# Kernel optimization log

Measured on AMD Instinct MI355X. Metric: run time of the kernel, lower is better.

## Reference

```python
import jax, jax.numpy as jnp
import numpy as np

N = 50000   # nodes
E = 400000  # edges
IN = 32     # in_channel
M = 64      # mid_channel
L = 3       # num_layers
EPS = 1e-5


def layer_norm(x, g, b):
    mu = jnp.mean(x, axis=-1, keepdims=True)
    var = jnp.mean((x - mu) ** 2, axis=-1, keepdims=True)
    return (x - mu) / jnp.sqrt(var + EPS) * g + b


def setup_inputs() -> dict:
    key = jax.random.key(0)
    ks = jax.random.split(key, 14)
    s = 0.05
    return {
        "x": jax.random.normal(ks[0], (N, IN), jnp.float32),
        "edge_index": jax.random.randint(ks[1], (2, E), 0, N, jnp.int64),
        # node encoder: Linear(IN->M) + LayerNorm(M)
        "enc_W": jax.random.normal(ks[2], (IN, M), jnp.float32) * s,
        "enc_b": jnp.zeros((M,), jnp.float32),
        "enc_g": jnp.ones((M,), jnp.float32),
        "enc_beta": jnp.zeros((M,), jnp.float32),
        # per-layer pre-norm
        "ln_g": jnp.ones((L, M), jnp.float32),
        "ln_b": jnp.zeros((L, M), jnp.float32),
        # SAGEConvV2 edge MLP: Linear(2M->2M) -> ReLU -> Linear(2M->M)
        "W1": jax.random.normal(ks[3], (L, 2 * M, 2 * M), jnp.float32) * s,
        "b1": jnp.zeros((L, 2 * M), jnp.float32),
        "W2": jax.random.normal(ks[4], (L, 2 * M, M), jnp.float32) * s,
        "b2": jnp.zeros((L, M), jnp.float32),
        # root weight lin_r: Linear(M->M, bias=False)
        "Wr": jax.random.normal(ks[5], (L, M, M), jnp.float32) * s,
    }


def reference(x, edge_index, enc_W, enc_b, enc_g, enc_beta,
              ln_g, ln_b, W1, b1, W2, b2, Wr):
    src = edge_index[0]  # x_j source nodes
    dst = edge_index[1]  # x_i target nodes (aggregation index)
    # node encoder
    x = layer_norm(x @ enc_W + enc_b, enc_g, enc_beta)
    # mean-aggregation denominator (in-degree, clamped to 1 like PyG scatter-mean)
    deg = jax.ops.segment_sum(jnp.ones((E,), x.dtype), dst, num_segments=N)
    deg = jnp.maximum(deg, 1.0)[:, None]
    for l in range(L):  # small fixed layer count
        # res+ block: norm -> act -> (dropout: identity in eval) -> conv -> residual
        h = jax.nn.relu(layer_norm(x, ln_g[l], ln_b[l]))
        # message: concat([x_i, x_j]) -> 2-layer MLP   [E, 2M] -> [E, M]
        msg = jnp.concatenate([h[dst], h[src]], axis=-1)
        msg = jax.nn.relu(msg @ W1[l] + b1[l]) @ W2[l] + b2[l]
        # scatter-mean aggregate at target nodes
        agg = jax.ops.segment_sum(msg, dst, num_segments=N) / deg
        # root weight
        h = agg + h @ Wr[l]
        x = x + h
    return x
```

## Files before the change

kernel.cpp:

```cpp
#include <hip/hip_runtime.h>
#include <hip/hip_bf16.h>

#define N_NODES 50000
#define N_EDGES 400000
#define IN_CH 32
#define EPS 1e-5f
#define SCAN_NB ((N_NODES + 1023) / 1024)
#define EL_CAP 384

#define HIST_B ((N_EDGES + 255) / 256)
#define WCT_TOT (3 * 320 * 64)
#define W2T_TOT (3 * 64 * 128)
#define RPK_B ((WCT_TOT + W2T_TOT + 255) / 256)
#define ENC_B ((N_NODES + 3) / 4)

typedef __attribute__((ext_vector_type(8))) short bh8;
typedef __attribute__((ext_vector_type(4))) float fx4;
typedef __attribute__((ext_vector_type(2))) float fx2;

static __device__ __forceinline__ unsigned int f2bf(float f) {
    __hip_bfloat16 h = __float2bfloat16(f);
    return (unsigned int)*(unsigned short*)&h;
}
static __device__ __forceinline__ unsigned short f2bfu(float f) {
    __hip_bfloat16 h = __float2bfloat16(f);
    return *(unsigned short*)&h;
}
static __device__ __forceinline__ float bflo(unsigned int u) { return __uint_as_float(u << 16); }

__global__ __launch_bounds__(256) void setup_kernel(
    const int* __restrict__ ei, int* __restrict__ cnt,
    const float* __restrict__ W1, const float* __restrict__ Wr,
    const float* __restrict__ W2,
    unsigned short* __restrict__ WcT, unsigned short* __restrict__ W2T,
    const float* __restrict__ x, const float* __restrict__ encW,
    const float* __restrict__ encb, const float* __restrict__ encg,
    const float* __restrict__ encbeta, float* __restrict__ xout) {
    int b = blockIdx.x;
    if (b < HIST_B) {
        int e = b * 256 + threadIdx.x;
        if (e < N_EDGES) atomicAdd(&cnt[ei[N_EDGES + e]], 1);
        return;
    }
    b -= HIST_B;
    if (b < RPK_B) {
        int t = b * 256 + threadIdx.x;
        if (t < WCT_TOT) {
            int l = t / (320 * 64);
            int rem = t % (320 * 64);
            int j = rem / 64, c = rem % 64;
            float v;
            if (j < 128)      v = W1[(l * 128 + c) * 128 + j];
            else if (j < 256) v = W1[(l * 128 + 64 + c) * 128 + (j - 128)];
            else              v = Wr[(l * 64 + c) * 64 + (j - 256)];
            WcT[t] = f2bfu(v);
        } else if (t < WCT_TOT + W2T_TOT) {
            int t2 = t - WCT_TOT;
            int l = t2 / 8192, rem = t2 % 8192;
            int n = rem / 128, k = rem % 128;
            W2T[t2] = f2bfu(W2[l * 8192 + k * 64 + n]);
        }
        return;
    }
    b -= RPK_B;
    __shared__ float wlds[IN_CH * 64];
    for (int t = threadIdx.x; t < IN_CH * 64; t += 256) wlds[t] = encW[t];
    __syncthreads();
    int lane = threadIdx.x & 63;
    int node = b * 4 + (threadIdx.x >> 6);
    if (node >= N_NODES) return;
    float xv = (lane < IN_CH) ? x[node * IN_CH + lane] : 0.f;
    float acc = encb[lane];
    #pragma unroll
    for (int c = 0; c < IN_CH; ++c) {
        float xc = __shfl(xv, c, 64);
        acc += xc * wlds[c * 64 + lane];
    }
    float s = acc;
    for (int off = 32; off; off >>= 1) s += __shfl_xor(s, off, 64);
    float mu = s * (1.f / 64.f);
    float d = acc - mu;
    float q = d * d;
    for (int off = 32; off; off >>= 1) q += __shfl_xor(q, off, 64);
    float r = rsqrtf(q * (1.f / 64.f) + EPS);
    xout[node * 64 + lane] = d * r * encg[lane] + encbeta[lane];
}

__global__ __launch_bounds__(1024) void scan1_kernel(const int* __restrict__ cnt,
                                                     int* __restrict__ exw,
                                                     int* __restrict__ bsum) {
    int b = blockIdx.x, t = threadIdx.x;
    int i = b * 1024 + t;
    int v = (i < N_NODES) ? cnt[i] : 0;
    int lane = t & 63, w = t >> 6;
    int s = v;
    #pragma unroll
    for (int off = 1; off < 64; off <<= 1) {
        int u = __shfl_up(s, off, 64);
        if (lane >= off) s += u;
    }
    __shared__ int ws[16];
    if (lane == 63) ws[w] = s;
    __syncthreads();
    if (t < 16) {
        int sv = ws[t];
        #pragma unroll
        for (int off = 1; off < 16; off <<= 1) {
            int u = __shfl_up(sv, off, 64);
            if (lane >= off) sv += u;
        }
        ws[t] = sv;
    }
    __syncthreads();
    int prefix = (w > 0) ? ws[w - 1] : 0;
    int incl = s + prefix;
    if (i < N_NODES) exw[i] = incl - v;
    if (t == 1023) bsum[b] = incl;
}

__global__ __launch_bounds__(1024) void scan3_kernel(const int* __restrict__ exw,
                                                     const int* __restrict__ bsum,
                                                     int* __restrict__ rp,
                                                     int* __restrict__ cnt) {
    __shared__ int pfx;
    __shared__ int total;
    int b = blockIdx.x, t = threadIdx.x;
    if (t < 64) {
        int v = (t < SCAN_NB) ? bsum[t] : 0;
        #pragma unroll
        for (int off = 1; off < 64; off <<= 1) {
            int u = __shfl_up(v, off, 64);
            if (t >= off) v += u;
        }
        if (b == 0 && t == 0) pfx = 0;
        if (b > 0 && t == b - 1) pfx = v;
        if (t == SCAN_NB - 1) total = v;
    }
    __syncthreads();
    int i = b * 1024 + t;
    if (i < N_NODES) {
        rp[i] = exw[i] + pfx;
        cnt[i] = 0;
    }
    if (b == 0 && t == 0) rp[N_NODES] = total;
}

__global__ void fill_kernel(const int* __restrict__ ei, const int* __restrict__ rp,
                            int* __restrict__ cur, int* __restrict__ el) {
    int e = blockIdx.x * 256 + threadIdx.x;
    if (e < N_EDGES) {
        int d = ei[N_EDGES + e];
        int p = atomicAdd(&cur[d], 1);
        el[rp[d] + p] = ei[e];
    }
}

__global__ __launch_bounds__(256, 8) void fused8_kernel(
    float* __restrict__ x,
    const unsigned char* __restrict__ A8I, const unsigned char* __restrict__ B8I,
    const unsigned short* __restrict__ W2T, const float* __restrict__ b2,
    const int* __restrict__ rp, const int* __restrict__ el,
    const float* __restrict__ g, const float* __restrict__ bvec,
    const unsigned short* __restrict__ WcT, const float* __restrict__ b1,
    unsigned char* __restrict__ A8O, unsigned char* __restrict__ B8O,
    unsigned short* __restrict__ Rbf, int mode) {
    __shared__ float bufF[1088];
    __shared__ unsigned int slds[16][68];
    __shared__ int el_lds[EL_CAP];
    __shared__ int rp_lds[17];
    int tid = threadIdx.x;
    int lane = tid & 63, wid = tid >> 6;
    int l15 = lane & 15, g4 = lane >> 4;
    int base = blockIdx.x * 16;
    unsigned int* hU = (unsigned int*)bufF;
    int n = tid >> 4, sq = tid & 15;

    int col = wid * 16 + l15;
    int nd_l = base + g4 * 4;

    if (mode != 0) {
        if (tid < 17) rp_lds[tid] = rp[min(base + tid, N_NODES)];
        __syncthreads();
        int e0 = rp_lds[0];
        int nE = rp_lds[16] - e0;
        bool inl = (nE <= EL_CAP);
        if (inl) for (int t = tid; t < nE; t += 256) el_lds[t] = el[e0 + t];

        int nd_g = base + n;
        float av[8], acc[8];
        {
            uint2 a0 = *(const uint2*)(A8I + (size_t)min(nd_g, N_NODES - 1) * 128 + sq * 8);
            fx2 d0 = __builtin_amdgcn_cvt_pk_f32_fp8((int)a0.x, false);
            fx2 d1 = __builtin_amdgcn_cvt_pk_f32_fp8((int)a0.x, true);
            fx2 d2 = __builtin_amdgcn_cvt_pk_f32_fp8((int)a0.y, false);
            fx2 d3 = __builtin_amdgcn_cvt_pk_f32_fp8((int)a0.y, true);
            av[0] = d0.x; av[1] = d0.y; av[2] = d1.x; av[3] = d1.y;
            av[4] = d2.x; av[5] = d2.y; av[6] = d3.x; av[7] = d3.y;
        }
        #pragma unroll
        for (int i = 0; i < 8; ++i) acc[i] = 0.f;

        float xpre[4], rpre[4];
        #pragma unroll
        for (int r = 0; r < 4; ++r) {
            int nd = min(nd_l + r, N_NODES - 1);
            xpre[r] = x[(size_t)nd * 64 + col];
            rpre[r] = bflo((unsigned int)Rbf[(size_t)nd * 64 + col]);
        }
        __syncthreads();

        int es = rp_lds[n] - e0, ee = rp_lds[n + 1] - e0;
        int e2 = es;
        int cn = ee - e2; if (cn > 8) cn = 8;
        uint2 bufv[8];
        #pragma unroll
        for (int j = 0; j < 8; ++j)
            if (j < cn) {
                int src = inl ? el_lds[e2 + j] : el[e0 + e2 + j];
                bufv[j] = *(const uint2*)(B8I + (size_t)src * 128 + sq * 8);
            }
        while (cn > 0) {
            #pragma unroll
            for (int j = 0; j < 8; ++j)
                if (j < cn) {
                    fx2 f0 = __builtin_amdgcn_cvt_pk_f32_fp8((int)bufv[j].x, false);
                    fx2 f1 = __builtin_amdgcn_cvt_pk_f32_fp8((int)bufv[j].x, true);
                    fx2 f2 = __builtin_amdgcn_cvt_pk_f32_fp8((int)bufv[j].y, false);
                    fx2 f3 = __builtin_amdgcn_cvt_pk_f32_fp8((int)bufv[j].y, true);
                    acc[0] += fmaxf(av[0] + f0.x, 0.f);
                    acc[1] += fmaxf(av[1] + f0.y, 0.f);
                    acc[2] += fmaxf(av[2] + f1.x, 0.f);
                    acc[3] += fmaxf(av[3] + f1.y, 0.f);
                    acc[4] += fmaxf(av[4] + f2.x, 0.f);
                    acc[5] += fmaxf(av[5] + f2.y, 0.f);
                    acc[6] += fmaxf(av[6] + f3.x, 0.f);
                    acc[7] += fmaxf(av[7] + f3.y, 0.f);
                }
            e2 += cn;
            cn = ee - e2; if (cn > 8) cn = 8;
            #pragma unroll
            for (int j = 0; j < 8; ++j)
                if (j < cn) {
                    int src = inl ? el_lds[e2 + j] : el[e0 + e2 + j];
                    bufv[j] = *(const uint2*)(B8I + (size_t)src * 128 + sq * 8);
                }
        }
        #pragma unroll
        for (int jj = 0; jj < 4; ++jj)
            slds[n][sq * 4 + jj] = f2bf(acc[2 * jj]) | (f2bf(acc[2 * jj + 1]) << 16);
        __syncthreads();

        bh8 sa[4];
        #pragma unroll
        for (int ks = 0; ks < 4; ++ks)
            sa[ks] = *(const bh8*)&slds[l15][ks * 16 + g4 * 4];
        fx4 accm = (fx4){0.f, 0.f, 0.f, 0.f};
        #pragma unroll
        for (int ks = 0; ks < 4; ++ks) {
            bh8 bf = *(const bh8*)(W2T + ((size_t)(wid * 16 + l15) * 128 + ks * 32 + g4 * 8));
            accm = __builtin_amdgcn_mfma_f32_16x16x32_bf16(sa[ks], bf, accm, 0, 0, 0);
        }
        float b2c = b2[col];
        #pragma unroll
        for (int r = 0; r < 4; ++r) {
            int lcl = g4 * 4 + r;
            int cv = rp_lds[lcl + 1] - rp_lds[lcl];
            float inv = cv > 0 ? 1.f / (float)cv : 0.f;
            float msk = cv > 0 ? 1.f : 0.f;
            int nd = nd_l + r;
            float xn = xpre[r] + accm[r] * inv + b2c * msk + rpre[r];
            if (nd < N_NODES) x[(size_t)nd * 64 + col] = xn;
            if (mode == 1) bufF[lcl * 68 + col] = xn;
        }
        if (mode == 2) return;
        __syncthreads();
    }

    {
        float vv[4];
        if (mode == 0) {
            int nd = base + n;
            float4 v0 = make_float4(0.f, 0.f, 0.f, 0.f);
            if (nd < N_NODES) v0 = ((const float4*)(x + (size_t)nd * 64))[sq];
            vv[0] = v0.x; vv[1] = v0.y; vv[2] = v0.z; vv[3] = v0.w;
        } else {
            #pragma unroll
            for (int i = 0; i < 4; ++i) vv[i] = bufF[n * 68 + sq * 4 + i];
        }
        float s = vv[0] + vv[1] + vv[2] + vv[3];
        s += __shfl_xor(s, 1, 16);
        s += __shfl_xor(s, 2, 16);
        s += __shfl_xor(s, 4, 16);
        s += __shfl_xor(s, 8, 16);
        float mu = s * (1.f / 64.f);
        float q = 0.f;
        #pragma unroll
        for (int i = 0; i < 4; ++i) { float d = vv[i] - mu; q += d * d; }
        q += __shfl_xor(q, 1, 16);
        q += __shfl_xor(q, 2, 16);
        q += __shfl_xor(q, 4, 16);
        q += __shfl_xor(q, 8, 16);
        float rs = rsqrtf(q * (1.f / 64.f) + EPS);
        float4 gg = *(const float4*)&g[sq * 4];
        float4 bb = *(const float4*)&bvec[sq * 4];
        float gv[4] = {gg.x, gg.y, gg.z, gg.w};
        float bv[4] = {bb.x, bb.y, bb.z, bb.w};
        __syncthreads();
        #pragma unroll
        for (int jj = 0; jj < 2; ++jj) {
            float h0 = fmaxf((vv[2 * jj] - mu) * rs * gv[2 * jj] + bv[2 * jj], 0.f);
            float h1 = fmaxf((vv[2 * jj + 1] - mu) * rs * gv[2 * jj + 1] + bv[2 * jj + 1], 0.f);
            hU[n * 33 + sq * 2 + jj] = f2bf(h0) | (f2bf(h1) << 16);
        }
    }
    __syncthreads();

    bh8 a2[2];
    #pragma unroll
    for (int ks = 0; ks < 2; ++ks)
        a2[ks] = *(const bh8*)&hU[l15 * 33 + ks * 16 + g4 * 4];
    int ndg = base + g4 * 4;
    #pragma unroll
    for (int nn = 0; nn < 5; ++nn) {
        int nb = wid * 5 + nn;
        fx4 c = (fx4){0.f, 0.f, 0.f, 0.f};
        #pragma unroll
        for (int ks = 0; ks < 2; ++ks) {
            bh8 bf = *(const bh8*)(WcT + ((size_t)(nb * 16 + l15) * 64 + ks * 32 + g4 * 8));
            c = __builtin_amdgcn_mfma_f32_16x16x32_bf16(a2[ks], bf, c, 0, 0, 0);
        }
        int colw = nb * 16 + l15;
        #pragma unroll
        for (int r = 0; r < 4; ++r) {
            int nd = ndg + r;
            if (nd >= N_NODES) continue;
            float v = c[r];
            if (colw < 128) {
                unsigned int p = __builtin_amdgcn_cvt_pk_fp8_f32(v + b1[colw], 0.f, 0, false);
                A8O[(size_t)nd * 128 + colw] = (unsigned char)(p & 0xFF);
            } else if (colw < 256) {
                unsigned int p = __builtin_amdgcn_cvt_pk_fp8_f32(v, 0.f, 0, false);
                B8O[(size_t)nd * 128 + (colw - 128)] = (unsigned char)(p & 0xFF);
            } else {
                Rbf[(size_t)nd * 64 + (colw - 256)] = f2bfu(v);
            }
        }
    }
}

extern "C" void kernel_launch(void* const* d_in, const int* in_sizes, int n_in,
                              void* d_out, int out_size, void* d_ws, size_t ws_size,
                              hipStream_t stream) {
    const float* x       = (const float*)d_in[0];
    const int*   ei      = (const int*)d_in[1];
    const float* encW    = (const float*)d_in[2];
    const float* encb    = (const float*)d_in[3];
    const float* encg    = (const float*)d_in[4];
    const float* encbeta = (const float*)d_in[5];
    const float* lng     = (const float*)d_in[6];
    const float* lnb     = (const float*)d_in[7];
    const float* W1      = (const float*)d_in[8];
    const float* b1      = (const float*)d_in[9];
    const float* W2      = (const float*)d_in[10];
    const float* b2      = (const float*)d_in[11];
    const float* Wr      = (const float*)d_in[12];
    float* xout = (float*)d_out;

    char* ws = (char*)d_ws;
    size_t off = 0;
    auto alloc = [&](size_t bytes) -> void* {
        void* p = ws + off;
        off += (bytes + 255) & ~(size_t)255;
        return p;
    };
    unsigned short* WcT  = (unsigned short*)alloc(3 * 320 * 64 * sizeof(unsigned short));
    unsigned short* W2T  = (unsigned short*)alloc(3 * 64 * 128 * sizeof(unsigned short));
    unsigned char*  A80  = (unsigned char*)alloc((size_t)N_NODES * 128);
    unsigned char*  A81  = (unsigned char*)alloc((size_t)N_NODES * 128);
    unsigned char*  B80  = (unsigned char*)alloc((size_t)N_NODES * 128);
    unsigned char*  B81  = (unsigned char*)alloc((size_t)N_NODES * 128);
    unsigned short* Rbf  = (unsigned short*)alloc((size_t)N_NODES * 64 * sizeof(unsigned short));
    int*            cnt  = (int*)alloc(N_NODES * sizeof(int));
    int*            rp   = (int*)alloc((N_NODES + 1) * sizeof(int));
    int*            el   = (int*)alloc(N_EDGES * sizeof(int));
    int*            exw  = (int*)alloc(N_NODES * sizeof(int));
    int*            bsum = (int*)alloc(SCAN_NB * sizeof(int));

    hipMemsetAsync(cnt, 0, N_NODES * sizeof(int), stream);
    setup_kernel<<<HIST_B + RPK_B + ENC_B, 256, 0, stream>>>(
        ei, cnt, W1, Wr, W2, WcT, W2T, x, encW, encb, encg, encbeta, xout);
    scan1_kernel<<<SCAN_NB, 1024, 0, stream>>>(cnt, exw, bsum);
    scan3_kernel<<<SCAN_NB, 1024, 0, stream>>>(exw, bsum, rp, cnt);
    fill_kernel<<<(N_EDGES + 255) / 256, 256, 0, stream>>>(ei, rp, cnt, el);

    int gblocks = (N_NODES + 15) / 16;
    fused8_kernel<<<gblocks, 256, 0, stream>>>(
        xout, A80, B80, W2T, b2, rp, el, lng, lnb,
        WcT, b1, A80, B80, Rbf, 0);
    fused8_kernel<<<gblocks, 256, 0, stream>>>(
        xout, A80, B80, W2T, b2, rp, el, lng + 64, lnb + 64,
        WcT + (size_t)1 * 320 * 64, b1 + 128, A81, B81, Rbf, 1);
    fused8_kernel<<<gblocks, 256, 0, stream>>>(
        xout, A81, B81, W2T + (size_t)1 * 64 * 128, b2 + 64, rp, el, lng + 128, lnb + 128,
        WcT + (size_t)2 * 320 * 64, b1 + 256, A80, B80, Rbf, 1);
    fused8_kernel<<<gblocks, 256, 0, stream>>>(
        xout, A80, B80, W2T + (size_t)2 * 64 * 128, b2 + 128, rp, el, lng, lnb,
        WcT, b1, A81, B81, Rbf, 2);
}
```

Baseline: 229.5 us.

## Use MFMA for node encoder and drop LDS edge-list staging in fused kernel

The node encoder now converts inputs and weights to bf16 and computes 16 nodes per wave with MFMA, so a block covers 64 nodes instead of 4, replacing scalar shuffle-FMA loops. The fused layer kernel no longer stages row pointers and the edge list in LDS behind barriers. It reads rp and el directly from global memory and prefetches source indices before the gathers. Bounds checks on node indices are removed because N is divisible by 16, and the encoder's bf16 rounding slightly lowers precision.

```diff
diff --git a/kernel.cpp b/kernel.cpp
--- a/kernel.cpp
+++ b/kernel.cpp
@@ -6,13 +6,12 @@
 #define IN_CH 32
 #define EPS 1e-5f
 #define SCAN_NB ((N_NODES + 1023) / 1024)
-#define EL_CAP 384
 
 #define HIST_B ((N_EDGES + 255) / 256)
 #define WCT_TOT (3 * 320 * 64)
 #define W2T_TOT (3 * 64 * 128)
 #define RPK_B ((WCT_TOT + W2T_TOT + 255) / 256)
-#define ENC_B ((N_NODES + 3) / 4)
+#define ENC_B ((N_NODES + 63) / 64)
 
 typedef __attribute__((ext_vector_type(8))) short bh8;
 typedef __attribute__((ext_vector_type(4))) float fx4;
@@ -63,27 +62,63 @@
         return;
     }
     b -= RPK_B;
-    __shared__ float wlds[IN_CH * 64];
-    for (int t = threadIdx.x; t < IN_CH * 64; t += 256) wlds[t] = encW[t];
+    __shared__ unsigned short wT[64 * 32];
+    int tid = threadIdx.x;
+    for (int t = tid; t < IN_CH * 64; t += 256) {
+        int k = t >> 6, c = t & 63;
+        wT[c * 32 + k] = f2bfu(encW[t]);
+    }
     __syncthreads();
-    int lane = threadIdx.x & 63;
-    int node = b * 4 + (threadIdx.x >> 6);
-    if (node >= N_NODES) return;
-    float xv = (lane < IN_CH) ? x[node * IN_CH + lane] : 0.f;
-    float acc = encb[lane];
-    #pragma unroll
-    for (int c = 0; c < IN_CH; ++c) {
-        float xc = __shfl(xv, c, 64);
-        acc += xc * wlds[c * 64 + lane];
-    }
-    float s = acc;
-    for (int off = 32; off; off >>= 1) s += __shfl_xor(s, off, 64);
-    float mu = s * (1.f / 64.f);
-    float d = acc - mu;
-    float q = d * d;
-    for (int off = 32; off; off >>= 1) q += __shfl_xor(q, off, 64);
-    float r = rsqrtf(q * (1.f / 64.f) + EPS);
-    xout[node * 64 + lane] = d * r * encg[lane] + encbeta[lane];
+    int lane = tid & 63, wid = tid >> 6;
+    int l15 = lane & 15, g4 = lane >> 4;
+    int node0 = b * 64 + wid * 16;
+    int arow = min(node0 + l15, N_NODES - 1);
+    float4 xa = *(const float4*)(x + (size_t)arow * 32 + g4 * 8);
+    float4 xb = *(const float4*)(x + (size_t)arow * 32 + g4 * 8 + 4);
+    bh8 af;
+    af[0] = (short)f2bfu(xa.x); af[1] = (short)f2bfu(xa.y);
+    af[2] = (short)f2bfu(xa.z); af[3] = (short)f2bfu(xa.w);
+    af[4] = (short)f2bfu(xb.x); af[5] = (short)f2bfu(xb.y);
+    af[6] = (short)f2bfu(xb.z); af[7] = (short)f2bfu(xb.w);
+    float cb[4], gvv[4], bvv[4];
+    fx4 cf[4];
+    #pragma unroll
+    for (int nb = 0; nb < 4; ++nb) {
+        int cc = nb * 16 + l15;
+        cb[nb] = encb[cc]; gvv[nb] = encg[cc]; bvv[nb] = encbeta[cc];
+        bh8 bf = *(const bh8*)&wT[(nb * 16 + l15) * 32 + g4 * 8];
+        cf[nb] = __builtin_amdgcn_mfma_f32_16x16x32_bf16(
+            af, bf, (fx4){0.f, 0.f, 0.f, 0.f}, 0, 0, 0);
+    }
+    float vals[4][4];
+    #pragma unroll
+    for (int nb = 0; nb < 4; ++nb)
+        #pragma unroll
+        for (int r = 0; r < 4; ++r) vals[nb][r] = cf[nb][r] + cb[nb];
+    #pragma unroll
+    for (int r = 0; r < 4; ++r) {
+        float s = vals[0][r] + vals[1][r] + vals[2][r] + vals[3][r];
+        s += __shfl_xor(s, 1, 16);
+        s += __shfl_xor(s, 2, 16);
+        s += __shfl_xor(s, 4, 16);
+        s += __shfl_xor(s, 8, 16);
+        float mu = s * (1.f / 64.f);
+        float q = 0.f;
+        #pragma unroll
+        for (int nb = 0; nb < 4; ++nb) { float d = vals[nb][r] - mu; q += d * d; }
+        q += __shfl_xor(q, 1, 16);
+        q += __shfl_xor(q, 2, 16);
+        q += __shfl_xor(q, 4, 16);
+        q += __shfl_xor(q, 8, 16);
+        float rs = rsqrtf(q * (1.f / 64.f) + EPS);
+        int nd = node0 + g4 * 4 + r;
+        if (nd < N_NODES) {
+            #pragma unroll
+            for (int nb = 0; nb < 4; ++nb)
+                xout[(size_t)nd * 64 + nb * 16 + l15] =
+                    (vals[nb][r] - mu) * rs * gvv[nb] + bvv[nb];
+        }
+    }
 }
 
 __global__ __launch_bounds__(1024) void scan1_kernel(const int* __restrict__ cnt,
@@ -155,7 +190,7 @@
     }
 }
 
-__global__ __launch_bounds__(256, 8) void fused8_kernel(
+__global__ __launch_bounds__(256, 8) void fused9_kernel(
     float* __restrict__ x,
     const unsigned char* __restrict__ A8I, const unsigned char* __restrict__ B8I,
     const unsigned short* __restrict__ W2T, const float* __restrict__ b2,
@@ -166,8 +201,6 @@
     unsigned short* __restrict__ Rbf, int mode) {
     __shared__ float bufF[1088];
     __shared__ unsigned int slds[16][68];
-    __shared__ int el_lds[EL_CAP];
-    __shared__ int rp_lds[17];
     int tid = threadIdx.x;
     int lane = tid & 63, wid = tid >> 6;
     int l15 = lane & 15, g4 = lane >> 4;
@@ -179,17 +212,22 @@
     int nd_l = base + g4 * 4;
 
     if (mode != 0) {
-        if (tid < 17) rp_lds[tid] = rp[min(base + tid, N_NODES)];
-        __syncthreads();
-        int e0 = rp_lds[0];
-        int nE = rp_lds[16] - e0;
-        bool inl = (nE <= EL_CAP);
-        if (inl) for (int t = tid; t < nE; t += 256) el_lds[t] = el[e0 + t];
-
-        int nd_g = base + n;
+        int nd_n = base + n;
+        int es = rp[nd_n], ee = rp[nd_n + 1];
+        uint2 a0 = *(const uint2*)(A8I + (size_t)nd_n * 128 + sq * 8);
+        float xpre[4], rpre[4];
+        int rpv[5];
+        #pragma unroll
+        for (int r = 0; r < 4; ++r) {
+            int nd = nd_l + r;
+            xpre[r] = x[(size_t)nd * 64 + col];
+            rpre[r] = bflo((unsigned int)Rbf[(size_t)nd * 64 + col]);
+        }
+        #pragma unroll
+        for (int r = 0; r < 5; ++r) rpv[r] = rp[nd_l + r];
+
         float av[8], acc[8];
         {
-            uint2 a0 = *(const uint2*)(A8I + (size_t)min(nd_g, N_NODES - 1) * 128 + sq * 8);
             fx2 d0 = __builtin_amdgcn_cvt_pk_f32_fp8((int)a0.x, false);
             fx2 d1 = __builtin_amdgcn_cvt_pk_f32_fp8((int)a0.x, true);
             fx2 d2 = __builtin_amdgcn_cvt_pk_f32_fp8((int)a0.y, false);
@@ -200,25 +238,15 @@
         #pragma unroll
         for (int i = 0; i < 8; ++i) acc[i] = 0.f;
 
-        float xpre[4], rpre[4];
-        #pragma unroll
-        for (int r = 0; r < 4; ++r) {
-            int nd = min(nd_l + r, N_NODES - 1);
-            xpre[r] = x[(size_t)nd * 64 + col];
-            rpre[r] = bflo((unsigned int)Rbf[(size_t)nd * 64 + col]);
-        }
-        __syncthreads();
-
-        int es = rp_lds[n] - e0, ee = rp_lds[n + 1] - e0;
         int e2 = es;
         int cn = ee - e2; if (cn > 8) cn = 8;
+        int srcs[8];
         uint2 bufv[8];
         #pragma unroll
+        for (int j = 0; j < 8; ++j) if (j < cn) srcs[j] = el[e2 + j];
+        #pragma unroll
         for (int j = 0; j < 8; ++j)
-            if (j < cn) {
-                int src = inl ? el_lds[e2 + j] : el[e0 + e2 + j];
-                bufv[j] = *(const uint2*)(B8I + (size_t)src * 128 + sq * 8);
-            }
+            if (j < cn) bufv[j] = *(const uint2*)(B8I + (size_t)srcs[j] * 128 + sq * 8);
         while (cn > 0) {
             #pragma unroll
             for (int j = 0; j < 8; ++j)
@@ -239,11 +267,10 @@
             e2 += cn;
             cn = ee - e2; if (cn > 8) cn = 8;
             #pragma unroll
+            for (int j = 0; j < 8; ++j) if (j < cn) srcs[j] = el[e2 + j];
+            #pragma unroll
             for (int j = 0; j < 8; ++j)
-                if (j < cn) {
-                    int src = inl ? el_lds[e2 + j] : el[e0 + e2 + j];
-                    bufv[j] = *(const uint2*)(B8I + (size_t)src * 128 + sq * 8);
-                }
+                if (j < cn) bufv[j] = *(const uint2*)(B8I + (size_t)srcs[j] * 128 + sq * 8);
         }
         #pragma unroll
         for (int jj = 0; jj < 4; ++jj)
@@ -263,14 +290,13 @@
         float b2c = b2[col];
         #pragma unroll
         for (int r = 0; r < 4; ++r) {
-            int lcl = g4 * 4 + r;
-            int cv = rp_lds[lcl + 1] - rp_lds[lcl];
+            int cv = rpv[r + 1] - rpv[r];
             float inv = cv > 0 ? 1.f / (float)cv : 0.f;
             float msk = cv > 0 ? 1.f : 0.f;
             int nd = nd_l + r;
             float xn = xpre[r] + accm[r] * inv + b2c * msk + rpre[r];
-            if (nd < N_NODES) x[(size_t)nd * 64 + col] = xn;
-            if (mode == 1) bufF[lcl * 68 + col] = xn;
+            x[(size_t)nd * 64 + col] = xn;
+            if (mode == 1) bufF[(g4 * 4 + r) * 68 + col] = xn;
         }
         if (mode == 2) return;
         __syncthreads();
@@ -280,8 +306,7 @@
         float vv[4];
         if (mode == 0) {
             int nd = base + n;
-            float4 v0 = make_float4(0.f, 0.f, 0.f, 0.f);
-            if (nd < N_NODES) v0 = ((const float4*)(x + (size_t)nd * 64))[sq];
+            float4 v0 = ((const float4*)(x + (size_t)nd * 64))[sq];
             vv[0] = v0.x; vv[1] = v0.y; vv[2] = v0.z; vv[3] = v0.w;
         } else {
             #pragma unroll
@@ -333,7 +358,6 @@
         #pragma unroll
         for (int r = 0; r < 4; ++r) {
             int nd = ndg + r;
-            if (nd >= N_NODES) continue;
             float v = c[r];
             if (colw < 128) {
                 unsigned int p = __builtin_amdgcn_cvt_pk_fp8_f32(v + b1[colw], 0.f, 0, false);
@@ -394,16 +418,16 @@
     fill_kernel<<<(N_EDGES + 255) / 256, 256, 0, stream>>>(ei, rp, cnt, el);
 
     int gblocks = (N_NODES + 15) / 16;
-    fused8_kernel<<<gblocks, 256, 0, stream>>>(
+    fused9_kernel<<<gblocks, 256, 0, stream>>>(
         xout, A80, B80, W2T, b2, rp, el, lng, lnb,
         WcT, b1, A80, B80, Rbf, 0);
-    fused8_kernel<<<gblocks, 256, 0, stream>>>(
+    fused9_kernel<<<gblocks, 256, 0, stream>>>(
         xout, A80, B80, W2T, b2, rp, el, lng + 64, lnb + 64,
         WcT + (size_t)1 * 320 * 64, b1 + 128, A81, B81, Rbf, 1);
-    fused8_kernel<<<gblocks, 256, 0, stream>>>(
+    fused9_kernel<<<gblocks, 256, 0, stream>>>(
         xout, A81, B81, W2T + (size_t)1 * 64 * 128, b2 + 64, rp, el, lng + 128, lnb + 128,
         WcT + (size_t)2 * 320 * 64, b1 + 256, A80, B80, Rbf, 1);
-    fused8_kernel<<<gblocks, 256, 0, stream>>>(
+    fused9_kernel<<<gblocks, 256, 0, stream>>>(
         xout, A80, B80, W2T + (size_t)2 * 64 * 128, b2 + 128, rp, el, lng, lnb,
         WcT, b1, A81, B81, Rbf, 2);
 }
```

Result: slower. 280.7 us (+22.3%).
